# Kernel optimization log

Hardware: AMD Instinct MI355X
Metric: run time of the kernel (lower is better)

The kernel has to match this reference:

```python
import jax, jax.numpy as jnp
import numpy as np

B, N, M = 8, 4096, 4096


def setup_inputs() -> dict:
    key = jax.random.key(0)
    k1, k2 = jax.random.split(key)
    tar = jax.random.normal(k1, (B, N, 3), dtype=jnp.float32)
    src = jax.random.normal(k2, (B, M, 3), dtype=jnp.float32)
    return {"tar": tar, "src": src}


def reference(tar, src):
    # diff: [b, n, m, 3]; dist: [b, n, m] Euclidean norm
    diff = tar[:, :, None, :] - src[:, None, :, :]
    dist = jnp.sqrt(jnp.sum(diff * diff, axis=-1))
    # complete: for each target point, min over source points, mean over n -> [b]
    complete = jnp.mean(jnp.min(dist, axis=2), axis=1)
    # accuracy: for each source point, min over target points, mean over m -> [b]
    accuracy = jnp.mean(jnp.min(dist, axis=1), axis=1)
    # reduction='mean' over batch axis
    complete = jnp.mean(complete, axis=-1)
    accuracy = jnp.mean(accuracy, axis=-1)
    chamfer = 0.5 * (complete + accuracy)
    return (accuracy, complete, chamfer)
```

## Files before the change

### kernel.cpp

```cpp
#include <hip/hip_runtime.h>
#include <math.h>

#define B_ 8
#define BIGF 3.4e38f


__global__ __launch_bounds__(256) void pack_kernel(
    const float* __restrict__ tar, const float* __restrict__ src,
    float4* __restrict__ packT, float4* __restrict__ packS,
    unsigned int* __restrict__ minarr, float* __restrict__ outp,
    int N, int M)
{
    const int i = blockIdx.x * 256 + threadIdx.x;
    const int nT = B_ * N, nS = B_ * M;
    if (i < nT) {
        float x = tar[3 * i], y = tar[3 * i + 1], z = tar[3 * i + 2];
        packT[i] = make_float4(x, y, z, fmaf(x, x, fmaf(y, y, z * z)));
    } else if (i < nT + nS) {
        int j = i - nT;
        float x = src[3 * j], y = src[3 * j + 1], z = src[3 * j + 2];
        packS[j] = make_float4(x, y, z, fmaf(x, x, fmaf(y, y, z * z)));
    }
    if (i < nT + nS) minarr[i] = 0x7F800000u;
    if (i < 3) outp[i] = 0.f;
}

template <int QPT, int CHUNK>
__global__ __launch_bounds__(256) void minsq_kernel(
    const float4* __restrict__ packT, const float4* __restrict__ packS,
    unsigned int* __restrict__ minarr, int N, int M)
{
    const int z   = blockIdx.z;
    const int dir = (z >= B_) ? 1 : 0;
    const int b   = dir ? (z - B_) : z;
    const float4* __restrict__ qry = dir ? packS : packT;
    const float4* __restrict__ pts = dir ? packT : packS;
    const int K = dir ? M : N;
    const int L = dir ? N : M;
    unsigned int* __restrict__ out =
        minarr + (dir ? (size_t)B_ * N : (size_t)0) + (size_t)b * K;

    const int base = blockIdx.y * CHUNK;
    if (base >= L) return;
    const int cnt = min(CHUNK, L - base);

    __shared__ float4 sp[CHUNK];
    const float4* __restrict__ psrc = pts + (size_t)b * L + base;
    const int t = threadIdx.x;
    for (int i = t; i < cnt; i += 256) sp[i] = psrc[i];
    __syncthreads();

    const int qbase = blockIdx.x * (256 * QPT);
    float qx2[QPT], qy2[QPT], qz2[QPT], qw[QPT], mn[QPT];
#pragma unroll
    for (int k = 0; k < QPT; ++k) {
        int qi = qbase + k * 256 + t;
        if (qi < K) {
            float4 q = qry[(size_t)b * K + qi];
            qx2[k] = -2.f * q.x; qy2[k] = -2.f * q.y; qz2[k] = -2.f * q.z;
            qw[k] = q.w;
        } else {
            qx2[k] = 0.f; qy2[k] = 0.f; qz2[k] = 0.f; qw[k] = 0.f;
        }
        mn[k] = BIGF;
    }

    if (cnt == CHUNK) {
#pragma unroll 4
        for (int j = 0; j < CHUNK; j += 2) {
            float4 p0 = sp[j];
            float4 p1 = sp[j + 1];
#pragma unroll
            for (int k = 0; k < QPT; ++k) {
                float d0 = fmaf(qx2[k], p0.x, fmaf(qy2[k], p0.y,
                           fmaf(qz2[k], p0.z, p0.w)));
                float d1 = fmaf(qx2[k], p1.x, fmaf(qy2[k], p1.y,
                           fmaf(qz2[k], p1.z, p1.w)));
                mn[k] = fminf(mn[k], fminf(d0, d1));
            }
        }
    } else {
        int j = 0;
        for (; j + 1 < cnt; j += 2) {
            float4 p0 = sp[j];
            float4 p1 = sp[j + 1];
#pragma unroll
            for (int k = 0; k < QPT; ++k) {
                float d0 = fmaf(qx2[k], p0.x, fmaf(qy2[k], p0.y,
                           fmaf(qz2[k], p0.z, p0.w)));
                float d1 = fmaf(qx2[k], p1.x, fmaf(qy2[k], p1.y,
                           fmaf(qz2[k], p1.z, p1.w)));
                mn[k] = fminf(mn[k], fminf(d0, d1));
            }
        }
        if (j < cnt) {
            float4 p0 = sp[j];
#pragma unroll
            for (int k = 0; k < QPT; ++k) {
                float d0 = fmaf(qx2[k], p0.x, fmaf(qy2[k], p0.y,
                           fmaf(qz2[k], p0.z, p0.w)));
                mn[k] = fminf(mn[k], d0);
            }
        }
    }

#pragma unroll
    for (int k = 0; k < QPT; ++k) {
        int qi = qbase + k * 256 + t;
        if (qi < K) {
            float d2 = fmaxf(mn[k] + qw[k], 0.f);
            atomicMin(&out[qi], __float_as_uint(d2));
        }
    }
}

__global__ __launch_bounds__(256) void reduce_kernel(
    const unsigned int* __restrict__ minarr, float* __restrict__ outp,
    int N, int M)
{
    const int nt = B_ * N, ns = B_ * M;
    const int gid = blockIdx.x * 256 + threadIdx.x;
    const int stride = gridDim.x * 256;
    float s_t = 0.f, s_s = 0.f;
    for (int i = gid; i < nt; i += stride)
        s_t += sqrtf(__uint_as_float(minarr[i]));
    for (int i = gid; i < ns; i += stride)
        s_s += sqrtf(__uint_as_float(minarr[nt + i]));
#pragma unroll
    for (int off = 32; off > 0; off >>= 1) {
        s_t += __shfl_down(s_t, off);
        s_s += __shfl_down(s_s, off);
    }
    __shared__ float rt[4], rs[4];
    const int wid = threadIdx.x >> 6, lid = threadIdx.x & 63;
    if (lid == 0) { rt[wid] = s_t; rs[wid] = s_s; }
    __syncthreads();
    if (threadIdx.x == 0) {
        float ct = (rt[0] + rt[1] + rt[2] + rt[3]) / (float)nt;
        float ac = (rs[0] + rs[1] + rs[2] + rs[3]) / (float)ns;
        atomicAdd(&outp[0], ac);
        atomicAdd(&outp[1], ct);
        atomicAdd(&outp[2], 0.5f * (ac + ct));
    }
}

extern "C" void kernel_launch(void* const* d_in, const int* in_sizes, int n_in,
                              void* d_out, int out_size, void* d_ws, size_t ws_size,
                              hipStream_t stream) {
    const float* tar = (const float*)d_in[0];
    const float* src = (const float*)d_in[1];
    const int N = in_sizes[0] / (B_ * 3);
    const int M = in_sizes[1] / (B_ * 3);

    float4* packT = (float4*)d_ws;
    float4* packS = packT + (size_t)B_ * N;
    unsigned int* minarr = (unsigned int*)(packS + (size_t)B_ * M);
    float* outp = (float*)d_out;

    pack_kernel<<<dim3((B_ * (N + M) + 255) / 256), dim3(256), 0, stream>>>(
        tar, src, packT, packS, minarr, outp, N, M);

    constexpr int QPT = 8, CHUNK = 128;
    const int KL = (N > M) ? N : M;
    const int gx = (KL + 256 * QPT - 1) / (256 * QPT);
    const int gy = (KL + CHUNK - 1) / CHUNK;
    dim3 grid(gx, gy, 2 * B_);
    minsq_kernel<QPT, CHUNK><<<grid, dim3(256), 0, stream>>>(
        packT, packS, minarr, N, M);

    reduce_kernel<<<dim3(32), dim3(256), 0, stream>>>(minarr, outp, N, M);
}
```

Baseline: 84.46 us.

## Fuse point packing into distance kernel and replace init kernel with memsets

Removes the separate pack kernel: the distance kernel now reads raw xyz triples, computes squared norms on the fly for both shared-memory points and per-thread queries, and the min array and outputs are initialised with async memsets. The inner loop gains a register double-buffer that loads the next pair of points from LDS before computing the current pair, and launch bounds request four blocks per CU. This saves a kernel launch and an intermediate buffer round trip, at the cost of strided 3-float loads and redundant norm computation in every block.

```diff
diff --git a/kernel.cpp b/kernel.cpp
--- a/kernel.cpp
+++ b/kernel.cpp
@@ -4,37 +4,16 @@
 #define B_ 8
 #define BIGF 3.4e38f
 
-
-__global__ __launch_bounds__(256) void pack_kernel(
+template <int QPT, int CHUNK>
+__global__ __launch_bounds__(256, 4) void minsq_kernel(
     const float* __restrict__ tar, const float* __restrict__ src,
-    float4* __restrict__ packT, float4* __restrict__ packS,
-    unsigned int* __restrict__ minarr, float* __restrict__ outp,
-    int N, int M)
-{
-    const int i = blockIdx.x * 256 + threadIdx.x;
-    const int nT = B_ * N, nS = B_ * M;
-    if (i < nT) {
-        float x = tar[3 * i], y = tar[3 * i + 1], z = tar[3 * i + 2];
-        packT[i] = make_float4(x, y, z, fmaf(x, x, fmaf(y, y, z * z)));
-    } else if (i < nT + nS) {
-        int j = i - nT;
-        float x = src[3 * j], y = src[3 * j + 1], z = src[3 * j + 2];
-        packS[j] = make_float4(x, y, z, fmaf(x, x, fmaf(y, y, z * z)));
-    }
-    if (i < nT + nS) minarr[i] = 0x7F800000u;
-    if (i < 3) outp[i] = 0.f;
-}
-
-template <int QPT, int CHUNK>
-__global__ __launch_bounds__(256) void minsq_kernel(
-    const float4* __restrict__ packT, const float4* __restrict__ packS,
     unsigned int* __restrict__ minarr, int N, int M)
 {
     const int z   = blockIdx.z;
     const int dir = (z >= B_) ? 1 : 0;
     const int b   = dir ? (z - B_) : z;
-    const float4* __restrict__ qry = dir ? packS : packT;
-    const float4* __restrict__ pts = dir ? packT : packS;
+    const float* __restrict__ qry = dir ? src : tar;
+    const float* __restrict__ pts = dir ? tar : src;
     const int K = dir ? M : N;
     const int L = dir ? N : M;
     unsigned int* __restrict__ out =
@@ -45,20 +24,24 @@
     const int cnt = min(CHUNK, L - base);
 
     __shared__ float4 sp[CHUNK];
-    const float4* __restrict__ psrc = pts + (size_t)b * L + base;
+    const float* __restrict__ p3 = pts + ((size_t)b * L + base) * 3;
     const int t = threadIdx.x;
-    for (int i = t; i < cnt; i += 256) sp[i] = psrc[i];
+    for (int i = t; i < cnt; i += 256) {
+        float x = p3[3 * i], y = p3[3 * i + 1], zc = p3[3 * i + 2];
+        sp[i] = make_float4(x, y, zc, fmaf(x, x, fmaf(y, y, zc * zc)));
+    }
     __syncthreads();
 
+    const float* __restrict__ q3 = qry + (size_t)b * K * 3;
     const int qbase = blockIdx.x * (256 * QPT);
     float qx2[QPT], qy2[QPT], qz2[QPT], qw[QPT], mn[QPT];
 #pragma unroll
     for (int k = 0; k < QPT; ++k) {
         int qi = qbase + k * 256 + t;
         if (qi < K) {
-            float4 q = qry[(size_t)b * K + qi];
-            qx2[k] = -2.f * q.x; qy2[k] = -2.f * q.y; qz2[k] = -2.f * q.z;
-            qw[k] = q.w;
+            float x = q3[3 * qi], y = q3[3 * qi + 1], zc = q3[3 * qi + 2];
+            qx2[k] = -2.f * x; qy2[k] = -2.f * y; qz2[k] = -2.f * zc;
+            qw[k] = fmaf(x, x, fmaf(y, y, zc * zc));
         } else {
             qx2[k] = 0.f; qy2[k] = 0.f; qz2[k] = 0.f; qw[k] = 0.f;
         }
@@ -66,18 +49,28 @@
     }
 
     if (cnt == CHUNK) {
-#pragma unroll 4
-        for (int j = 0; j < CHUNK; j += 2) {
-            float4 p0 = sp[j];
-            float4 p1 = sp[j + 1];
+        float4 c0 = sp[0], c1 = sp[1];
+#pragma unroll 2
+        for (int j = 0; j + 2 < CHUNK; j += 2) {
+            float4 n0 = sp[j + 2];
+            float4 n1 = sp[j + 3];
 #pragma unroll
             for (int k = 0; k < QPT; ++k) {
-                float d0 = fmaf(qx2[k], p0.x, fmaf(qy2[k], p0.y,
-                           fmaf(qz2[k], p0.z, p0.w)));
-                float d1 = fmaf(qx2[k], p1.x, fmaf(qy2[k], p1.y,
-                           fmaf(qz2[k], p1.z, p1.w)));
+                float d0 = fmaf(qx2[k], c0.x, fmaf(qy2[k], c0.y,
+                           fmaf(qz2[k], c0.z, c0.w)));
+                float d1 = fmaf(qx2[k], c1.x, fmaf(qy2[k], c1.y,
+                           fmaf(qz2[k], c1.z, c1.w)));
                 mn[k] = fminf(mn[k], fminf(d0, d1));
             }
+            c0 = n0; c1 = n1;
+        }
+#pragma unroll
+        for (int k = 0; k < QPT; ++k) {
+            float d0 = fmaf(qx2[k], c0.x, fmaf(qy2[k], c0.y,
+                       fmaf(qz2[k], c0.z, c0.w)));
+            float d1 = fmaf(qx2[k], c1.x, fmaf(qy2[k], c1.y,
+                       fmaf(qz2[k], c1.z, c1.w)));
+            mn[k] = fminf(mn[k], fminf(d0, d1));
         }
     } else {
         int j = 0;
@@ -152,13 +145,12 @@
     const int N = in_sizes[0] / (B_ * 3);
     const int M = in_sizes[1] / (B_ * 3);
 
-    float4* packT = (float4*)d_ws;
-    float4* packS = packT + (size_t)B_ * N;
-    unsigned int* minarr = (unsigned int*)(packS + (size_t)B_ * M);
+    unsigned int* minarr = (unsigned int*)d_ws;
     float* outp = (float*)d_out;
 
-    pack_kernel<<<dim3((B_ * (N + M) + 255) / 256), dim3(256), 0, stream>>>(
-        tar, src, packT, packS, minarr, outp, N, M);
+    hipMemsetAsync(minarr, 0xFF, (size_t)B_ * (N + M) * sizeof(unsigned int),
+                   stream);
+    hipMemsetAsync(outp, 0, 3 * sizeof(float), stream);
 
     constexpr int QPT = 8, CHUNK = 128;
     const int KL = (N > M) ? N : M;
@@ -166,7 +158,7 @@
     const int gy = (KL + CHUNK - 1) / CHUNK;
     dim3 grid(gx, gy, 2 * B_);
     minsq_kernel<QPT, CHUNK><<<grid, dim3(256), 0, stream>>>(
-        packT, packS, minarr, N, M);
+        tar, src, minarr, N, M);
 
     reduce_kernel<<<dim3(32), dim3(256), 0, stream>>>(minarr, outp, N, M);
 }
```

Result: no change. 84.76 us (+0.4%).
